# Optimization experiments

Measured on AMD Instinct MI355X. Metric: run time of the kernel, lower is better.

The kernel has to match this reference:

```python
import jax, jax.numpy as jnp
import numpy as np

BLOCK_SIZE = 256
EMB = 384
HEAD = 64
B = 256
T = 256

def setup_inputs() -> dict:
    key = jax.random.key(0)
    k1, k2, k3, k4 = jax.random.split(key, 4)
    x = jax.random.normal(k1, (B, T, EMB), dtype=jnp.float32)
    # torch Linear(no bias) default init ~ U(-1/sqrt(in), 1/sqrt(in)); use scaled normal
    s = 1.0 / np.sqrt(EMB)
    Wq = jax.random.normal(k2, (EMB, HEAD), dtype=jnp.float32) * s
    Wk = jax.random.normal(k3, (EMB, HEAD), dtype=jnp.float32) * s
    Wv = jax.random.normal(k4, (EMB, HEAD), dtype=jnp.float32) * s
    return {"x": x, "Wq": Wq, "Wk": Wk, "Wv": Wv}

def reference(x, Wq, Wk, Wv):
    Bb, Tt, C = x.shape
    q = jnp.einsum('btc,ch->bth', x, Wq)
    k = jnp.einsum('btc,ch->bth', x, Wk)
    v = jnp.einsum('btc,ch->bth', x, Wv)
    # NOTE: source scales by C**-0.5 where C = embedding dim (384), not head_size
    scores = jnp.einsum('bth,bsh->bts', q, k) * (C ** -0.5)  # [B,T,T]
    causal = jnp.tril(jnp.ones((Tt, Tt), dtype=bool))
    scores = jnp.where(causal, scores, -jnp.inf)
    weights = jax.nn.softmax(scores, axis=-1)
    # dropout is identity in eval mode (reference baseline)
    out = jnp.einsum('bts,bsh->bth', weights, v)
    return out
```

## Files before the change

kernel.cpp:

```cpp
#include <hip/hip_runtime.h>
#include <hip/hip_bf16.h>
#include <cstdint>
#include <cstddef>

#define B_DIM 256
#define T_DIM 256
#define EMB   384
#define HEAD  64
#define QS    (B_DIM * T_DIM * HEAD)

typedef __attribute__((ext_vector_type(8))) short bf16x8;
typedef __attribute__((ext_vector_type(4))) float f32x4;
typedef __attribute__((ext_vector_type(4))) unsigned int u32x4;

__device__ __forceinline__ unsigned short f2bf(float f) {
    union { float f; unsigned int u; } v; v.f = f;
    unsigned int r = v.u + 0x7fffu + ((v.u >> 16) & 1u);
    return (unsigned short)(r >> 16);
}

__device__ __forceinline__ unsigned int pkbf(float a, float b) {
#if __has_builtin(__builtin_amdgcn_cvt_pk_bf16_f32)
    typedef __attribute__((ext_vector_type(2))) __bf16 bf16x2_t;
    bf16x2_t r = __builtin_amdgcn_cvt_pk_bf16_f32(a, b);
    return *(unsigned int*)&r;
#else
    return (unsigned)f2bf(a) | ((unsigned)f2bf(b) << 16);
#endif
}

__global__ void wprep_kernel(const float* __restrict__ Wq, const float* __restrict__ Wk,
                             const float* __restrict__ Wv, unsigned short* __restrict__ Wb) {
    int g = blockIdx.x * blockDim.x + threadIdx.x;
    if (g >= 9216) return;
    int kkstep = g / 1536, rem = g - kkstep * 1536;
    int r = rem >> 3, cs = rem & 7, c = cs ^ (r & 7);
    const float* W = (r < 64) ? Wq : (r < 128) ? Wk : Wv;
    int h = r & 63;
#pragma unroll
    for (int e = 0; e < 8; ++e) {
        int k = kkstep * 64 + c * 8 + e;
        Wb[(size_t)g * 8 + e] = f2bf(W[k * HEAD + h]);
    }
}

__global__ __launch_bounds__(256) void qkv_kernel(const float* __restrict__ x,
                                                  const unsigned short* __restrict__ Wb,
                                                  unsigned short* __restrict__ qkv) {
    __shared__ unsigned short Xs[128][72];
    __shared__ unsigned short Ws[192 * 64];
    const int tid = threadIdx.x;
    const int w = tid >> 6, lane = tid & 63, qd = lane >> 4, l15 = lane & 15;
    const int mh = w >> 1, nh = w & 1;
    const int m0 = blockIdx.x * 128;

    f32x4 acc[4][6];
#pragma unroll
    for (int mt = 0; mt < 4; ++mt)
#pragma unroll
        for (int nt = 0; nt < 6; ++nt) acc[mt][nt] = (f32x4){0.f, 0.f, 0.f, 0.f};

    for (int kk = 0; kk < 6; ++kk) {
#pragma unroll
        for (int s = 0; s < 6; ++s) {
            int idx = s * 256 + w * 64;
            const unsigned short* gp = Wb + (size_t)(kk * 1536 + idx + lane) * 8;
            unsigned short* lp = Ws + (size_t)idx * 8;
            __builtin_amdgcn_global_load_lds(
                (const __attribute__((address_space(1))) unsigned int*)gp,
                (__attribute__((address_space(3))) unsigned int*)lp, 16, 0, 0);
        }
#pragma unroll
        for (int s = 0; s < 8; ++s) {
            int i = tid + 256 * s;
            int row = i >> 4, c4 = (i & 15) << 2;
            const float4 vx = *(const float4*)(x + (size_t)(m0 + row) * EMB + kk * 64 + c4);
            *(uint2*)&Xs[row][c4] = make_uint2(pkbf(vx.x, vx.y), pkbf(vx.z, vx.w));
        }
        __syncthreads();
#pragma unroll
        for (int kb = 0; kb < 2; ++kb) {
            bf16x8 a[4], bb[6];
#pragma unroll
            for (int mt = 0; mt < 4; ++mt)
                a[mt] = *(const bf16x8*)&Xs[64 * mh + 16 * mt + l15][32 * kb + 8 * qd];
#pragma unroll
            for (int nt = 0; nt < 6; ++nt) {
                int n = 96 * nh + 16 * nt + l15;
                bb[nt] = *(const bf16x8*)&Ws[n * 64 + (((4 * kb + qd) ^ (n & 7)) << 3)];
            }
#pragma unroll
            for (int mt = 0; mt < 4; ++mt)
#pragma unroll
                for (int nt = 0; nt < 6; ++nt)
                    acc[mt][nt] = __builtin_amdgcn_mfma_f32_16x16x32_bf16(a[mt], bb[nt], acc[mt][nt], 0, 0, 0);
        }
        __syncthreads();
    }
#pragma unroll
    for (int nt = 0; nt < 6; ++nt) {
        int n = 96 * nh + 16 * nt + l15;
        int arr = n >> 6, h = n & 63;
        unsigned short* dst = qkv + (size_t)arr * QS + h;
#pragma unroll
        for (int mt = 0; mt < 4; ++mt)
#pragma unroll
            for (int reg = 0; reg < 4; ++reg) {
                int row = m0 + 64 * mh + 16 * mt + 4 * qd + reg;
                dst[(size_t)row * HEAD] = f2bf(acc[mt][nt][reg]);
            }
    }
}

__global__ __launch_bounds__(512, 1) void attn_kernel(const unsigned short* __restrict__ qkv,
                                                      float* __restrict__ out) {
    __shared__ unsigned short ks[256][72];
    __shared__ unsigned short vT[64][264];
    __shared__ unsigned short Ps[8][16][72];
    const int tid = threadIdx.x;
    const int w = tid >> 6, lane = tid & 63, qd = lane >> 4, l15 = lane & 15;
    const int b = blockIdx.x;
    const unsigned short* qb = qkv + (size_t)b * T_DIM * HEAD;
    const unsigned short* kb = qkv + (size_t)QS + (size_t)b * T_DIM * HEAD;
    const unsigned short* vb = qkv + 2 * (size_t)QS + (size_t)b * T_DIM * HEAD;

#pragma unroll
    for (int s = 0; s < 4; ++s) {
        int i = tid + 512 * s;
        int row = i >> 3, ch = (i & 7) << 3;
        *(u32x4*)&ks[row][ch] = *(const u32x4*)(kb + row * HEAD + ch);
    }
#pragma unroll
    for (int s = 0; s < 2; ++s) {
        int i = tid + 512 * s;
        int t = i >> 2, d0 = (i & 3) << 4;
        union { u32x4 v; unsigned short u[8]; } t0, t1;
        t0.v = *(const u32x4*)(vb + t * HEAD + d0);
        t1.v = *(const u32x4*)(vb + t * HEAD + d0 + 8);
#pragma unroll
        for (int e = 0; e < 8; ++e) { vT[d0 + e][t] = t0.u[e]; vT[d0 + 8 + e][t] = t1.u[e]; }
    }
    const int tiles[2] = { w, 15 - w };
    bf16x8 aq[2][2];
#pragma unroll
    for (int ti = 0; ti < 2; ++ti)
#pragma unroll
        for (int kbi = 0; kbi < 2; ++kbi)
            aq[ti][kbi] = *(const bf16x8*)(qb + (16 * tiles[ti] + l15) * HEAD + 32 * kbi + 8 * qd);
    __syncthreads();

    f32x4 O[2][4];
    float l[2][4];
#pragma unroll
    for (int ti = 0; ti < 2; ++ti) {
#pragma unroll
        for (int dn = 0; dn < 4; ++dn) O[ti][dn] = (f32x4){0.f, 0.f, 0.f, 0.f};
#pragma unroll
        for (int reg = 0; reg < 4; ++reg) l[ti][reg] = 0.f;
    }

    const float cExp = 1.4426950408889634f / 19.595917942265423f;

#pragma unroll
    for (int ti = 0; ti < 2; ++ti) {
        const int t = tiles[ti];
        for (int jc = 0; jc <= (t >> 2); ++jc) {
            const int ntmax = min(3, t - 4 * jc);
            f32x4 S[4];
#pragma unroll
            for (int nt = 0; nt < 4; ++nt) {
                if (nt <= ntmax) {
                    bf16x8 b0 = *(const bf16x8*)&ks[64 * jc + 16 * nt + l15][8 * qd];
                    bf16x8 b1 = *(const bf16x8*)&ks[64 * jc + 16 * nt + l15][32 + 8 * qd];
                    f32x4 s = __builtin_amdgcn_mfma_f32_16x16x32_bf16(aq[ti][0], b0, (f32x4){0.f,0.f,0.f,0.f}, 0, 0, 0);
                    s = __builtin_amdgcn_mfma_f32_16x16x32_bf16(aq[ti][1], b1, s, 0, 0, 0);
                    S[nt] = s;
                }
            }
#pragma unroll
            for (int nt = 0; nt < 4; ++nt) {
#pragma unroll
                for (int reg = 0; reg < 4; ++reg) {
                    float p = 0.0f;
                    if (nt <= ntmax) {
                        p = exp2f(S[nt][reg] * cExp);
                        if (4 * jc + nt == t && (l15 > 4 * qd + reg)) p = 0.0f;
                    }
                    l[ti][reg] += p;
                    Ps[w][4 * qd + reg][16 * nt + l15] = f2bf(p);
                }
            }
            bf16x8 ap0 = *(const bf16x8*)&Ps[w][l15][8 * qd];
            bf16x8 ap1 = *(const bf16x8*)&Ps[w][l15][32 + 8 * qd];
#pragma unroll
            for (int dn = 0; dn < 4; ++dn) {
                bf16x8 bv0 = *(const bf16x8*)&vT[16 * dn + l15][64 * jc + 8 * qd];
                bf16x8 bv1 = *(const bf16x8*)&vT[16 * dn + l15][64 * jc + 32 + 8 * qd];
                O[ti][dn] = __builtin_amdgcn_mfma_f32_16x16x32_bf16(ap0, bv0, O[ti][dn], 0, 0, 0);
                O[ti][dn] = __builtin_amdgcn_mfma_f32_16x16x32_bf16(ap1, bv1, O[ti][dn], 0, 0, 0);
            }
        }
    }

#pragma unroll
    for (int ti = 0; ti < 2; ++ti) {
#pragma unroll
        for (int reg = 0; reg < 4; ++reg) {
            float s = l[ti][reg];
            s += __shfl_xor(s, 1);
            s += __shfl_xor(s, 2);
            s += __shfl_xor(s, 4);
            s += __shfl_xor(s, 8);
            float inv = 1.0f / s;
            int row = 16 * tiles[ti] + 4 * qd + reg;
            float* dst = out + ((size_t)b * T_DIM + row) * HEAD;
#pragma unroll
            for (int dn = 0; dn < 4; ++dn)
                dst[16 * dn + l15] = O[ti][dn][reg] * inv;
        }
    }
}

extern "C" void kernel_launch(void* const* d_in, const int* in_sizes, int n_in,
                              void* d_out, int out_size, void* d_ws, size_t ws_size,
                              hipStream_t stream) {
    const float* x  = (const float*)d_in[0];
    const float* Wq = (const float*)d_in[1];
    const float* Wk = (const float*)d_in[2];
    const float* Wv = (const float*)d_in[3];
    float* out = (float*)d_out;

    unsigned short* qkv = (unsigned short*)d_ws;
    unsigned short* Wb  = qkv + 3 * (size_t)QS;

    wprep_kernel<<<36, 256, 0, stream>>>(Wq, Wk, Wv, Wb);
    qkv_kernel<<<(B_DIM * T_DIM) / 128, 256, 0, stream>>>(x, Wb, qkv);
    attn_kernel<<<B_DIM, 512, 0, stream>>>(qkv, out);
}
```

Before: 184.1 us.

## Fuse QKV projection and causal attention into one per-batch kernel

Merges the QKV projection and attention kernels into a single kernel with one 512-thread block per batch element. Q, K and V^T are written straight to LDS instead of round-tripping through global memory, which removes that traffic and one launch. The projection loop is also software-pipelined: weight tiles are double-buffered via async global-to-LDS loads and the next x chunk is prefetched into registers. The cost is one block per batch (256 blocks) with large LDS use and register pressure from acc plus the prefetch registers, which may limit occupancy.

```diff
diff --git a/kernel.cpp b/kernel.cpp
--- a/kernel.cpp
+++ b/kernel.cpp
@@ -7,7 +7,6 @@
 #define T_DIM 256
 #define EMB   384
 #define HEAD  64
-#define QS    (B_DIM * T_DIM * HEAD)
 
 typedef __attribute__((ext_vector_type(8))) short bf16x8;
 typedef __attribute__((ext_vector_type(4))) float f32x4;
@@ -44,15 +43,20 @@
     }
 }
 
-__global__ __launch_bounds__(256) void qkv_kernel(const float* __restrict__ x,
-                                                  const unsigned short* __restrict__ Wb,
-                                                  unsigned short* __restrict__ qkv) {
-    __shared__ unsigned short Xs[128][72];
-    __shared__ unsigned short Ws[192 * 64];
+__global__ __launch_bounds__(512, 2) void fused_kernel(const float* __restrict__ x,
+                                                       const unsigned short* __restrict__ Wb,
+                                                       float* __restrict__ out) {
+    __shared__ union SM {
+        struct { unsigned short Xs[256][72]; unsigned short Ws[2][12288]; } p1;
+        struct { unsigned short qs[256][72]; unsigned short ks[256][72];
+                 unsigned short vT[64][264]; unsigned short Ps[8][16][72]; } p2;
+    } sm;
+
     const int tid = threadIdx.x;
     const int w = tid >> 6, lane = tid & 63, qd = lane >> 4, l15 = lane & 15;
     const int mh = w >> 1, nh = w & 1;
-    const int m0 = blockIdx.x * 128;
+    const int b = blockIdx.x;
+    const float* xb = x + (size_t)b * T_DIM * EMB;
 
     f32x4 acc[4][6];
 #pragma unroll
@@ -60,34 +64,59 @@
 #pragma unroll
         for (int nt = 0; nt < 6; ++nt) acc[mt][nt] = (f32x4){0.f, 0.f, 0.f, 0.f};
 
+    float4 xr[8];
+#pragma unroll
+    for (int s = 0; s < 3; ++s) {
+        int idx = s * 512 + w * 64;
+        const unsigned short* gp = Wb + (size_t)(idx + lane) * 8;
+        unsigned short* lp = &sm.p1.Ws[0][idx * 8];
+        __builtin_amdgcn_global_load_lds(
+            (const __attribute__((address_space(1))) unsigned int*)gp,
+            (__attribute__((address_space(3))) unsigned int*)lp, 16, 0, 0);
+    }
+#pragma unroll
+    for (int s = 0; s < 8; ++s) {
+        int i = tid + 512 * s;
+        int row = i >> 4, c4 = (i & 15) << 2;
+        xr[s] = *(const float4*)(xb + (size_t)row * EMB + c4);
+    }
+
     for (int kk = 0; kk < 6; ++kk) {
-#pragma unroll
-        for (int s = 0; s < 6; ++s) {
-            int idx = s * 256 + w * 64;
-            const unsigned short* gp = Wb + (size_t)(kk * 1536 + idx + lane) * 8;
-            unsigned short* lp = Ws + (size_t)idx * 8;
-            __builtin_amdgcn_global_load_lds(
-                (const __attribute__((address_space(1))) unsigned int*)gp,
-                (__attribute__((address_space(3))) unsigned int*)lp, 16, 0, 0);
-        }
+        __syncthreads();
 #pragma unroll
         for (int s = 0; s < 8; ++s) {
-            int i = tid + 256 * s;
+            int i = tid + 512 * s;
             int row = i >> 4, c4 = (i & 15) << 2;
-            const float4 vx = *(const float4*)(x + (size_t)(m0 + row) * EMB + kk * 64 + c4);
-            *(uint2*)&Xs[row][c4] = make_uint2(pkbf(vx.x, vx.y), pkbf(vx.z, vx.w));
+            *(uint2*)&sm.p1.Xs[row][c4] = make_uint2(pkbf(xr[s].x, xr[s].y), pkbf(xr[s].z, xr[s].w));
         }
         __syncthreads();
+        if (kk < 5) {
+#pragma unroll
+            for (int s = 0; s < 3; ++s) {
+                int idx = s * 512 + w * 64;
+                const unsigned short* gp = Wb + (size_t)((kk + 1) * 1536 + idx + lane) * 8;
+                unsigned short* lp = &sm.p1.Ws[(kk + 1) & 1][idx * 8];
+                __builtin_amdgcn_global_load_lds(
+                    (const __attribute__((address_space(1))) unsigned int*)gp,
+                    (__attribute__((address_space(3))) unsigned int*)lp, 16, 0, 0);
+            }
+#pragma unroll
+            for (int s = 0; s < 8; ++s) {
+                int i = tid + 512 * s;
+                int row = i >> 4, c4 = (i & 15) << 2;
+                xr[s] = *(const float4*)(xb + (size_t)row * EMB + (kk + 1) * 64 + c4);
+            }
+        }
 #pragma unroll
         for (int kb = 0; kb < 2; ++kb) {
             bf16x8 a[4], bb[6];
 #pragma unroll
             for (int mt = 0; mt < 4; ++mt)
-                a[mt] = *(const bf16x8*)&Xs[64 * mh + 16 * mt + l15][32 * kb + 8 * qd];
+                a[mt] = *(const bf16x8*)&sm.p1.Xs[64 * mh + 16 * mt + l15][32 * kb + 8 * qd];
 #pragma unroll
             for (int nt = 0; nt < 6; ++nt) {
                 int n = 96 * nh + 16 * nt + l15;
-                bb[nt] = *(const bf16x8*)&Ws[n * 64 + (((4 * kb + qd) ^ (n & 7)) << 3)];
+                bb[nt] = *(const bf16x8*)&sm.p1.Ws[kk & 1][n * 64 + (((4 * kb + qd) ^ (n & 7)) << 3)];
             }
 #pragma unroll
             for (int mt = 0; mt < 4; ++mt)
@@ -95,59 +124,33 @@
                 for (int nt = 0; nt < 6; ++nt)
                     acc[mt][nt] = __builtin_amdgcn_mfma_f32_16x16x32_bf16(a[mt], bb[nt], acc[mt][nt], 0, 0, 0);
         }
-        __syncthreads();
-    }
+    }
+    __syncthreads();
+
 #pragma unroll
     for (int nt = 0; nt < 6; ++nt) {
         int n = 96 * nh + 16 * nt + l15;
         int arr = n >> 6, h = n & 63;
-        unsigned short* dst = qkv + (size_t)arr * QS + h;
 #pragma unroll
         for (int mt = 0; mt < 4; ++mt)
 #pragma unroll
             for (int reg = 0; reg < 4; ++reg) {
-                int row = m0 + 64 * mh + 16 * mt + 4 * qd + reg;
-                dst[(size_t)row * HEAD] = f2bf(acc[mt][nt][reg]);
-            }
-    }
-}
-
-__global__ __launch_bounds__(512, 1) void attn_kernel(const unsigned short* __restrict__ qkv,
-                                                      float* __restrict__ out) {
-    __shared__ unsigned short ks[256][72];
-    __shared__ unsigned short vT[64][264];
-    __shared__ unsigned short Ps[8][16][72];
-    const int tid = threadIdx.x;
-    const int w = tid >> 6, lane = tid & 63, qd = lane >> 4, l15 = lane & 15;
-    const int b = blockIdx.x;
-    const unsigned short* qb = qkv + (size_t)b * T_DIM * HEAD;
-    const unsigned short* kb = qkv + (size_t)QS + (size_t)b * T_DIM * HEAD;
-    const unsigned short* vb = qkv + 2 * (size_t)QS + (size_t)b * T_DIM * HEAD;
-
-#pragma unroll
-    for (int s = 0; s < 4; ++s) {
-        int i = tid + 512 * s;
-        int row = i >> 3, ch = (i & 7) << 3;
-        *(u32x4*)&ks[row][ch] = *(const u32x4*)(kb + row * HEAD + ch);
-    }
-#pragma unroll
-    for (int s = 0; s < 2; ++s) {
-        int i = tid + 512 * s;
-        int t = i >> 2, d0 = (i & 3) << 4;
-        union { u32x4 v; unsigned short u[8]; } t0, t1;
-        t0.v = *(const u32x4*)(vb + t * HEAD + d0);
-        t1.v = *(const u32x4*)(vb + t * HEAD + d0 + 8);
-#pragma unroll
-        for (int e = 0; e < 8; ++e) { vT[d0 + e][t] = t0.u[e]; vT[d0 + 8 + e][t] = t1.u[e]; }
-    }
+                int tok = 64 * mh + 16 * mt + 4 * qd + reg;
+                unsigned short val = f2bf(acc[mt][nt][reg]);
+                if (arr == 0)      sm.p2.qs[tok][h] = val;
+                else if (arr == 1) sm.p2.ks[tok][h] = val;
+                else               sm.p2.vT[h][tok] = val;
+            }
+    }
+    __syncthreads();
+
     const int tiles[2] = { w, 15 - w };
     bf16x8 aq[2][2];
 #pragma unroll
     for (int ti = 0; ti < 2; ++ti)
 #pragma unroll
         for (int kbi = 0; kbi < 2; ++kbi)
-            aq[ti][kbi] = *(const bf16x8*)(qb + (16 * tiles[ti] + l15) * HEAD + 32 * kbi + 8 * qd);
-    __syncthreads();
+            aq[ti][kbi] = *(const bf16x8*)&sm.p2.qs[16 * tiles[ti] + l15][32 * kbi + 8 * qd];
 
     f32x4 O[2][4];
     float l[2][4];
@@ -170,8 +173,8 @@
 #pragma unroll
             for (int nt = 0; nt < 4; ++nt) {
                 if (nt <= ntmax) {
-                    bf16x8 b0 = *(const bf16x8*)&ks[64 * jc + 16 * nt + l15][8 * qd];
-                    bf16x8 b1 = *(const bf16x8*)&ks[64 * jc + 16 * nt + l15][32 + 8 * qd];
+                    bf16x8 b0 = *(const bf16x8*)&sm.p2.ks[64 * jc + 16 * nt + l15][8 * qd];
+                    bf16x8 b1 = *(const bf16x8*)&sm.p2.ks[64 * jc + 16 * nt + l15][32 + 8 * qd];
                     f32x4 s = __builtin_amdgcn_mfma_f32_16x16x32_bf16(aq[ti][0], b0, (f32x4){0.f,0.f,0.f,0.f}, 0, 0, 0);
                     s = __builtin_amdgcn_mfma_f32_16x16x32_bf16(aq[ti][1], b1, s, 0, 0, 0);
                     S[nt] = s;
@@ -187,15 +190,15 @@
                         if (4 * jc + nt == t && (l15 > 4 * qd + reg)) p = 0.0f;
                     }
                     l[ti][reg] += p;
-                    Ps[w][4 * qd + reg][16 * nt + l15] = f2bf(p);
+                    sm.p2.Ps[w][4 * qd + reg][16 * nt + l15] = f2bf(p);
                 }
             }
-            bf16x8 ap0 = *(const bf16x8*)&Ps[w][l15][8 * qd];
-            bf16x8 ap1 = *(const bf16x8*)&Ps[w][l15][32 + 8 * qd];
+            bf16x8 ap0 = *(const bf16x8*)&sm.p2.Ps[w][l15][8 * qd];
+            bf16x8 ap1 = *(const bf16x8*)&sm.p2.Ps[w][l15][32 + 8 * qd];
 #pragma unroll
             for (int dn = 0; dn < 4; ++dn) {
-                bf16x8 bv0 = *(const bf16x8*)&vT[16 * dn + l15][64 * jc + 8 * qd];
-                bf16x8 bv1 = *(const bf16x8*)&vT[16 * dn + l15][64 * jc + 32 + 8 * qd];
+                bf16x8 bv0 = *(const bf16x8*)&sm.p2.vT[16 * dn + l15][64 * jc + 8 * qd];
+                bf16x8 bv1 = *(const bf16x8*)&sm.p2.vT[16 * dn + l15][64 * jc + 32 + 8 * qd];
                 O[ti][dn] = __builtin_amdgcn_mfma_f32_16x16x32_bf16(ap0, bv0, O[ti][dn], 0, 0, 0);
                 O[ti][dn] = __builtin_amdgcn_mfma_f32_16x16x32_bf16(ap1, bv1, O[ti][dn], 0, 0, 0);
             }
@@ -230,10 +233,8 @@
     const float* Wv = (const float*)d_in[3];
     float* out = (float*)d_out;
 
-    unsigned short* qkv = (unsigned short*)d_ws;
-    unsigned short* Wb  = qkv + 3 * (size_t)QS;
+    unsigned short* Wb = (unsigned short*)d_ws;
 
     wprep_kernel<<<36, 256, 0, stream>>>(Wq, Wk, Wv, Wb);
-    qkv_kernel<<<(B_DIM * T_DIM) / 128, 256, 0, stream>>>(x, Wb, qkv);
-    attn_kernel<<<B_DIM, 512, 0, stream>>>(qkv, out);
-}
+    fused_kernel<<<B_DIM, 512, 0, stream>>>(x, Wb, out);
+}
```

New measurement: 174.6 us. -5.1%, faster.
